# Performance work log

Hardware: AMD Instinct MI355X
Metric: run time of the kernel (lower is better)

Reference implementation:

```python
import jax, jax.numpy as jnp
import numpy as np

B = 16          # number of graphs in the batch (fixed for segment ops)
PTS = 4096      # points per graph
N = B * PTS
C = 256         # input feature channels
EPS = 1e-16     # PyG knn_interpolate eps


def setup_inputs() -> dict:
    key = jax.random.key(0)
    ks = jax.random.split(key, 12)
    x = jax.random.normal(ks[0], (N, C), dtype=jnp.float32)
    pos = jax.random.normal(ks[1], (N, 3), dtype=jnp.float32)
    x_skip = jax.random.normal(ks[2], (N, C), dtype=jnp.float32)
    pos_skip = jax.random.normal(ks[3], (N, 3), dtype=jnp.float32)
    # sorted segment ids, every graph populated
    batch = jnp.repeat(jnp.arange(B, dtype=jnp.int32), PTS)
    batch_skip = jnp.repeat(jnp.arange(B, dtype=jnp.int32), PTS)
    # MLP([C+3, 256, 512, 1024]) parameters (Linear + ReLU per layer)
    s = 0.02
    W1 = jax.random.normal(ks[4], (C + 3, 256), dtype=jnp.float32) * s
    b1 = jnp.zeros((256,), dtype=jnp.float32)
    W2 = jax.random.normal(ks[5], (256, 512), dtype=jnp.float32) * s
    b2 = jnp.zeros((512,), dtype=jnp.float32)
    W3 = jax.random.normal(ks[6], (512, 1024), dtype=jnp.float32) * s
    b3 = jnp.zeros((1024,), dtype=jnp.float32)
    return {"x": x, "pos": pos, "batch": batch, "x_skip": x_skip,
            "pos_skip": pos_skip, "batch_skip": batch_skip,
            "W1": W1, "b1": b1, "W2": W2, "b2": b2, "W3": W3, "b3": b3}


def reference(x, pos, batch, x_skip, pos_skip, batch_skip, W1, b1, W2, b2, W3, b3):
    # nn(cat([x, pos], dim=1)): 3-layer MLP with ReLU
    h = jnp.concatenate([x, pos], axis=1)            # [N, C+3]
    h = jax.nn.relu(h @ W1 + b1)                     # [N, 256]
    h = jax.nn.relu(h @ W2 + b2)                     # [N, 512]
    h = jax.nn.relu(h @ W3 + b3)                     # [N, 1024]
    # global_max_pool over each graph
    pooled = jax.ops.segment_max(h, batch, num_segments=B)  # [B, 1024]
    # knn_interpolate(pooled, origin-per-graph, pos_skip, k=3):
    # each graph contributes exactly ONE source point (the origin), so the
    # single in-batch neighbor gets inverse-distance weight that normalizes
    # to 1; written explicitly to mirror the PyG weighting math.
    d2 = jnp.sum(pos_skip * pos_skip, axis=1, keepdims=True)  # [Ns, 1] dist^2 to origin
    w = 1.0 / (d2 + EPS)
    gathered = pooled[batch_skip]                    # [Ns, 1024]
    interp = (w * gathered) / w                      # weights cancel -> gathered
    # cat with skip features
    out = jnp.concatenate([interp, x_skip], axis=1)  # [Ns, 1024 + C]
    return out
```

## Files before the change

### kernel.cpp

```cpp
#include <hip/hip_runtime.h>
#include <hip/hip_bf16.h>


typedef __attribute__((ext_vector_type(8))) short bf16x8;
typedef __attribute__((ext_vector_type(16))) float f32x16;

#define GLD_LDS16(src, dst) __builtin_amdgcn_global_load_lds( \
    (const __attribute__((address_space(1))) unsigned int*)(src), \
    (__attribute__((address_space(3))) unsigned int*)(dst), 16, 0, 0)

__device__ __forceinline__ unsigned short f2bf(float f) {
  unsigned int u = __float_as_uint(f);
  unsigned int r = (u + 0x7FFFu + ((u >> 16) & 1u)) >> 16;
  return (unsigned short)r;
}
__device__ __forceinline__ float bf2f(unsigned short h) {
  return __uint_as_float(((unsigned int)h) << 16);
}

__global__ void pack_a1(const float* __restrict__ x, const float* __restrict__ pos,
                        unsigned short* __restrict__ ah, unsigned short* __restrict__ al) {
  const int total = 65536 * 80;
  for (int idx = blockIdx.x * blockDim.x + threadIdx.x; idx < total;
       idx += gridDim.x * blockDim.x) {
    const int n = idx / 80;
    const int q = idx - n * 80;
    float4 v;
    if (q < 64) {
      v = ((const float4*)x)[(size_t)n * 64 + q];
    } else if (q == 64) {
      v.x = pos[(size_t)n * 3 + 0];
      v.y = pos[(size_t)n * 3 + 1];
      v.z = pos[(size_t)n * 3 + 2];
      v.w = 0.f;
    } else {
      v.x = v.y = v.z = v.w = 0.f;
    }
    ushort4 h, l;
    h.x = f2bf(v.x); l.x = f2bf(v.x - bf2f(h.x));
    h.y = f2bf(v.y); l.y = f2bf(v.y - bf2f(h.y));
    h.z = f2bf(v.z); l.z = f2bf(v.z - bf2f(h.z));
    h.w = f2bf(v.w); l.w = f2bf(v.w - bf2f(h.w));
    *(ushort4*)(ah + (size_t)n * 320 + q * 4) = h;
    *(ushort4*)(al + (size_t)n * 320 + q * 4) = l;
  }
}

__global__ void pack_w(const float* __restrict__ w, unsigned short* __restrict__ wh,
                       unsigned short* __restrict__ wl, int K, int Nout) {
  const int no = blockIdx.x;
  const int k = threadIdx.x;
  const int KP = blockDim.x;
  float v = (k < K) ? w[(size_t)k * Nout + no] : 0.f;
  unsigned short hi = f2bf(v);
  wh[(size_t)no * KP + k] = hi;
  wl[(size_t)no * KP + k] = f2bf(v - bf2f(hi));
}

__global__ void zero_pool(unsigned int* __restrict__ p) {
  p[blockIdx.x * 1024 + threadIdx.x] = 0u;
}

template<int KP, int NOUT, int MODE>
__global__ __launch_bounds__(256, 2)
void gemm_split(const unsigned short* __restrict__ gAh, const unsigned short* __restrict__ gAl,
                const unsigned short* __restrict__ gBh, const unsigned short* __restrict__ gBl,
                const float* __restrict__ bias,
                unsigned short* __restrict__ Ch, unsigned short* __restrict__ Cl,
                unsigned int* __restrict__ pooled, const int* __restrict__ batch) {
  constexpr int BM = 128, BN = 128, BK = 64;
  constexpr int NB = NOUT / BN;
  __shared__ unsigned short lds[4 * BM * BK];

  const int nwg = gridDim.x;
  const int bid = (blockIdx.x % 8) * (nwg / 8) + blockIdx.x / 8;
  const int bm = bid / NB, bn = bid % NB;
  const int r0 = bm * BM, c0 = bn * BN;
  const int tid = threadIdx.x;
  const int lane = tid & 63, wid = tid >> 6;
  const int wm = wid >> 1, wc = wid & 1;
  const int al31 = lane & 31, l5 = lane >> 5;
  const int swz = lane & 7, lr = lane >> 3;

  f32x16 acc[2][2] = {};

  const unsigned short* plane = (wid == 0) ? gAh : (wid == 1) ? gAl : (wid == 2) ? gBh : gBl;
  const int rb = (wid < 2) ? r0 : c0;
  unsigned short* sbase = lds + wid * (BM * BK);
  const unsigned short* gsrc0 = plane + (size_t)(rb + lr) * KP + ((swz ^ lr) << 3);
  unsigned short* ldst0 = sbase + lane * 8;

  for (int kt = 0; kt < KP / BK; ++kt) {
    {
      const unsigned short* s = gsrc0 + kt * BK;
      unsigned short* d = ldst0;
      #pragma unroll
      for (int t = 0; t < 16; ++t) {
        GLD_LDS16(s, d);
        s += 8 * KP;
        d += 512;
      }
    }
    __syncthreads();

    const unsigned short* sA_h = lds;
    const unsigned short* sA_l = lds + BM * BK;
    const unsigned short* sB_h = lds + 2 * BM * BK;
    const unsigned short* sB_l = lds + 3 * BM * BK;

    #pragma unroll
    for (int ks = 0; ks < BK / 16; ++ks) {
      bf16x8 fah[2], fal[2], fbh[2], fbl[2];
      const int cb = ks * 2 + l5;
      #pragma unroll
      for (int i = 0; i < 2; ++i) {
        const int arow = wm * 64 + i * 32 + al31;
        const int aoff = arow * BK + ((cb ^ (arow & 7)) << 3);
        fah[i] = *(const bf16x8*)(sA_h + aoff);
        fal[i] = *(const bf16x8*)(sA_l + aoff);
        const int brow = wc * 64 + i * 32 + al31;
        const int boff = brow * BK + ((cb ^ (brow & 7)) << 3);
        fbh[i] = *(const bf16x8*)(sB_h + boff);
        fbl[i] = *(const bf16x8*)(sB_l + boff);
      }
      #pragma unroll
      for (int i = 0; i < 2; ++i)
        #pragma unroll
        for (int j = 0; j < 2; ++j) {
          acc[i][j] = __builtin_amdgcn_mfma_f32_32x32x16_bf16(fah[i], fbh[j], acc[i][j], 0, 0, 0);
          acc[i][j] = __builtin_amdgcn_mfma_f32_32x32x16_bf16(fah[i], fbl[j], acc[i][j], 0, 0, 0);
          acc[i][j] = __builtin_amdgcn_mfma_f32_32x32x16_bf16(fal[i], fbh[j], acc[i][j], 0, 0, 0);
        }
    }
    __syncthreads();
  }

  if (MODE == 0) {
    #pragma unroll
    for (int i = 0; i < 2; ++i) {
      const int rbase = r0 + wm * 64 + i * 32 + 4 * l5;
      #pragma unroll
      for (int j = 0; j < 2; ++j) {
        const int col = c0 + wc * 64 + j * 32 + al31;
        const float bz = bias[col];
        #pragma unroll
        for (int r = 0; r < 16; ++r) {
          const int row = rbase + (r & 3) + 8 * (r >> 2);
          float v = fmaxf(acc[i][j][r] + bz, 0.f);
          unsigned short hi = f2bf(v);
          Ch[(size_t)row * NOUT + col] = hi;
          Cl[(size_t)row * NOUT + col] = f2bf(v - bf2f(hi));
        }
      }
    }
  } else {
    const int g = batch[r0];
    float* pb = (float*)lds;
    #pragma unroll
    for (int j = 0; j < 2; ++j) {
      const int colw = wc * 64 + j * 32 + al31;
      const float bz = bias[c0 + colw];
      float cm = 0.f;
      #pragma unroll
      for (int i = 0; i < 2; ++i)
        #pragma unroll
        for (int r = 0; r < 16; ++r)
          cm = fmaxf(cm, acc[i][j][r] + bz);
      cm = fmaxf(cm, __shfl_xor(cm, 32));
      if (l5 == 0) pb[wm * 128 + colw] = cm;
    }
    __syncthreads();
    if (tid < 128) {
      float m = fmaxf(pb[tid], pb[128 + tid]);
      atomicMax(pooled + (size_t)g * 1024 + c0 + tid, __float_as_uint(m));
    }
  }
}

__global__ void write_out(const float* __restrict__ pooled, const float* __restrict__ x_skip,
                          const int* __restrict__ batch_skip, float* __restrict__ out,
                          int N) {
  const int t = threadIdx.x;
  for (int n = blockIdx.x; n < N; n += gridDim.x) {
    const int g = batch_skip[n];
    const float4* ps = (const float4*)(pooled + (size_t)g * 1024);
    float4* o = (float4*)(out + (size_t)n * 1280);
    o[t] = ps[t];
    if (t < 64) {
      const float4* xs = (const float4*)(x_skip + (size_t)n * 256);
      o[256 + t] = xs[t];
    }
  }
}

extern "C" void kernel_launch(void* const* d_in, const int* in_sizes, int n_in,
                              void* d_out, int out_size, void* d_ws, size_t ws_size,
                              hipStream_t stream) {
  const float* x        = (const float*)d_in[0];
  const float* pos      = (const float*)d_in[1];
  const int*   batch    = (const int*)d_in[2];
  const float* x_skip   = (const float*)d_in[3];
  const int*   batch_sk = (const int*)d_in[5];
  const float* W1 = (const float*)d_in[6];
  const float* b1 = (const float*)d_in[7];
  const float* W2 = (const float*)d_in[8];
  const float* b2 = (const float*)d_in[9];
  const float* W3 = (const float*)d_in[10];
  const float* b3 = (const float*)d_in[11];
  float* out = (float*)d_out;

  char* ws = (char*)d_ws;
  unsigned short* a1h = (unsigned short*)(ws);
  unsigned short* a1l = (unsigned short*)(ws + 41943040);
  unsigned short* h2h = (unsigned short*)(ws);
  unsigned short* h2l = (unsigned short*)(ws + 67108864);
  size_t off = 134217728;
  unsigned short* h1h = (unsigned short*)(ws + off); off += 33554432;
  unsigned short* h1l = (unsigned short*)(ws + off); off += 33554432;
  unsigned short* w1h = (unsigned short*)(ws + off); off += 163840;
  unsigned short* w1l = (unsigned short*)(ws + off); off += 163840;
  unsigned short* w2h = (unsigned short*)(ws + off); off += 262144;
  unsigned short* w2l = (unsigned short*)(ws + off); off += 262144;
  unsigned short* w3h = (unsigned short*)(ws + off); off += 1048576;
  unsigned short* w3l = (unsigned short*)(ws + off); off += 1048576;
  unsigned int*  pooled = (unsigned int*)(ws + off);

  hipLaunchKernelGGL(pack_w, dim3(256),  dim3(320), 0, stream, W1, w1h, w1l, 259, 256);
  hipLaunchKernelGGL(pack_w, dim3(512),  dim3(256), 0, stream, W2, w2h, w2l, 256, 512);
  hipLaunchKernelGGL(pack_w, dim3(1024), dim3(512), 0, stream, W3, w3h, w3l, 512, 1024);
  hipLaunchKernelGGL(pack_a1, dim3(2048), dim3(256), 0, stream, x, pos, a1h, a1l);
  hipLaunchKernelGGL(zero_pool, dim3(16), dim3(1024), 0, stream, pooled);

  hipLaunchKernelGGL((gemm_split<320, 256, 0>), dim3(512 * 2), dim3(256), 0, stream,
                     a1h, a1l, w1h, w1l, b1, h1h, h1l,
                     (unsigned int*)nullptr, (const int*)nullptr);
  hipLaunchKernelGGL((gemm_split<256, 512, 0>), dim3(512 * 4), dim3(256), 0, stream,
                     h1h, h1l, w2h, w2l, b2, h2h, h2l,
                     (unsigned int*)nullptr, (const int*)nullptr);
  hipLaunchKernelGGL((gemm_split<512, 1024, 1>), dim3(512 * 8), dim3(256), 0, stream,
                     h2h, h2l, w3h, w3l, b3,
                     (unsigned short*)nullptr, (unsigned short*)nullptr, pooled, batch);

  hipLaunchKernelGGL(write_out, dim3(4096), dim3(256), 0, stream,
                     (const float*)pooled, x_skip, batch_sk, out, 65536);
}
```

Baseline: 771.1 us.

## Double-buffer split-bf16 GEMM LDS loads with 128x256 tiles and 512 threads

Restructures the split-precision GEMM kernel into a two-stage LDS double buffer: the next K-slice is loaded by global-to-LDS copies while the current slice feeds MFMA, which removes one barrier per iteration and overlaps memory with compute. The tile grows to 128x256 with BK=32 and 8 waves per block, so more output is computed per loaded A tile. The first layer's padded K also drops from 320 to 288 to cut wasted MFMA work. In exchange, per-iteration K depth is smaller, so there are more iterations and barriers, and LDS usage and register pressure rise.

New measurement: 820.8 us. 1.06x slower.

```diff
diff --git a/kernel.cpp b/kernel.cpp
--- a/kernel.cpp
+++ b/kernel.cpp
@@ -20,11 +20,11 @@
 
 __global__ void pack_a1(const float* __restrict__ x, const float* __restrict__ pos,
                         unsigned short* __restrict__ ah, unsigned short* __restrict__ al) {
-  const int total = 65536 * 80;
+  const int total = 65536 * 72;
   for (int idx = blockIdx.x * blockDim.x + threadIdx.x; idx < total;
        idx += gridDim.x * blockDim.x) {
-    const int n = idx / 80;
-    const int q = idx - n * 80;
+    const int n = idx / 72;
+    const int q = idx - n * 72;
     float4 v;
     if (q < 64) {
       v = ((const float4*)x)[(size_t)n * 64 + q];
@@ -41,8 +41,8 @@
     h.y = f2bf(v.y); l.y = f2bf(v.y - bf2f(h.y));
     h.z = f2bf(v.z); l.z = f2bf(v.z - bf2f(h.z));
     h.w = f2bf(v.w); l.w = f2bf(v.w - bf2f(h.w));
-    *(ushort4*)(ah + (size_t)n * 320 + q * 4) = h;
-    *(ushort4*)(al + (size_t)n * 320 + q * 4) = l;
+    *(ushort4*)(ah + (size_t)n * 288 + q * 4) = h;
+    *(ushort4*)(al + (size_t)n * 288 + q * 4) = l;
   }
 }
 
@@ -62,15 +62,17 @@
 }
 
 template<int KP, int NOUT, int MODE>
-__global__ __launch_bounds__(256, 2)
+__global__ __launch_bounds__(512, 2)
 void gemm_split(const unsigned short* __restrict__ gAh, const unsigned short* __restrict__ gAl,
                 const unsigned short* __restrict__ gBh, const unsigned short* __restrict__ gBl,
                 const float* __restrict__ bias,
                 unsigned short* __restrict__ Ch, unsigned short* __restrict__ Cl,
                 unsigned int* __restrict__ pooled, const int* __restrict__ batch) {
-  constexpr int BM = 128, BN = 128, BK = 64;
+  constexpr int BM = 128, BN = 256, BK = 32;
   constexpr int NB = NOUT / BN;
-  __shared__ unsigned short lds[4 * BM * BK];
+  constexpr int KT = KP / BK;
+  constexpr int BUF = 24576;
+  __shared__ unsigned short lds[2 * BUF];
 
   const int nwg = gridDim.x;
   const int bid = (blockIdx.x % 8) * (nwg / 8) + blockIdx.x / 8;
@@ -78,48 +80,60 @@
   const int r0 = bm * BM, c0 = bn * BN;
   const int tid = threadIdx.x;
   const int lane = tid & 63, wid = tid >> 6;
-  const int wm = wid >> 1, wc = wid & 1;
+  const int wm = wid >> 2, wn = wid & 3;
   const int al31 = lane & 31, l5 = lane >> 5;
-  const int swz = lane & 7, lr = lane >> 3;
+  const int lr = lane >> 2, swz = lane & 3;
 
   f32x16 acc[2][2] = {};
 
-  const unsigned short* plane = (wid == 0) ? gAh : (wid == 1) ? gAl : (wid == 2) ? gBh : gBl;
-  const int rb = (wid < 2) ? r0 : c0;
-  unsigned short* sbase = lds + wid * (BM * BK);
-  const unsigned short* gsrc0 = plane + (size_t)(rb + lr) * KP + ((swz ^ lr) << 3);
-  unsigned short* ldst0 = sbase + lane * 8;
-
-  for (int kt = 0; kt < KP / BK; ++kt) {
-    {
-      const unsigned short* s = gsrc0 + kt * BK;
-      unsigned short* d = ldst0;
-      #pragma unroll
-      for (int t = 0; t < 16; ++t) {
-        GLD_LDS16(s, d);
-        s += 8 * KP;
-        d += 512;
+  const unsigned short* src[6];
+  int dstoff[6];
+  #pragma unroll
+  for (int t = 0; t < 6; ++t) {
+    const int c = wid * 6 + t;
+    const unsigned short* pl; int rowb;
+    if (c < 8)       { pl = gAh; rowb = r0 + c * 16; }
+    else if (c < 16) { pl = gAl; rowb = r0 + (c - 8) * 16; }
+    else if (c < 32) { pl = gBh; rowb = c0 + (c - 16) * 16; }
+    else             { pl = gBl; rowb = c0 + (c - 32) * 16; }
+    src[t] = pl + (size_t)(rowb + lr) * KP + ((swz ^ (lr & 3)) << 3);
+    dstoff[t] = c * 512 + lane * 8;
+  }
+
+  #pragma unroll
+  for (int t = 0; t < 6; ++t) {
+    GLD_LDS16(src[t], lds + dstoff[t]);
+    src[t] += BK;
+  }
+  __syncthreads();
+
+  int cur = 0;
+  for (int kt = 0; kt < KT; ++kt) {
+    if (kt + 1 < KT) {
+      unsigned short* nb = lds + (cur ^ 1) * BUF;
+      #pragma unroll
+      for (int t = 0; t < 6; ++t) {
+        GLD_LDS16(src[t], nb + dstoff[t]);
+        src[t] += BK;
       }
     }
-    __syncthreads();
-
-    const unsigned short* sA_h = lds;
-    const unsigned short* sA_l = lds + BM * BK;
-    const unsigned short* sB_h = lds + 2 * BM * BK;
-    const unsigned short* sB_l = lds + 3 * BM * BK;
+    const unsigned short* sA_h = lds + cur * BUF;
+    const unsigned short* sA_l = sA_h + 4096;
+    const unsigned short* sB_h = sA_h + 8192;
+    const unsigned short* sB_l = sA_h + 16384;
 
     #pragma unroll
-    for (int ks = 0; ks < BK / 16; ++ks) {
+    for (int ks = 0; ks < 2; ++ks) {
       bf16x8 fah[2], fal[2], fbh[2], fbl[2];
       const int cb = ks * 2 + l5;
       #pragma unroll
       for (int i = 0; i < 2; ++i) {
         const int arow = wm * 64 + i * 32 + al31;
-        const int aoff = arow * BK + ((cb ^ (arow & 7)) << 3);
+        const int aoff = arow * BK + ((cb ^ (arow & 3)) << 3);
         fah[i] = *(const bf16x8*)(sA_h + aoff);
         fal[i] = *(const bf16x8*)(sA_l + aoff);
-        const int brow = wc * 64 + i * 32 + al31;
-        const int boff = brow * BK + ((cb ^ (brow & 7)) << 3);
+        const int brow = wn * 64 + i * 32 + al31;
+        const int boff = brow * BK + ((cb ^ (brow & 3)) << 3);
         fbh[i] = *(const bf16x8*)(sB_h + boff);
         fbl[i] = *(const bf16x8*)(sB_l + boff);
       }
@@ -133,6 +147,7 @@
         }
     }
     __syncthreads();
+    cur ^= 1;
   }
 
   if (MODE == 0) {
@@ -141,7 +156,7 @@
       const int rbase = r0 + wm * 64 + i * 32 + 4 * l5;
       #pragma unroll
       for (int j = 0; j < 2; ++j) {
-        const int col = c0 + wc * 64 + j * 32 + al31;
+        const int col = c0 + wn * 64 + j * 32 + al31;
         const float bz = bias[col];
         #pragma unroll
         for (int r = 0; r < 16; ++r) {
@@ -158,7 +173,7 @@
     float* pb = (float*)lds;
     #pragma unroll
     for (int j = 0; j < 2; ++j) {
-      const int colw = wc * 64 + j * 32 + al31;
+      const int colw = wn * 64 + j * 32 + al31;
       const float bz = bias[c0 + colw];
       float cm = 0.f;
       #pragma unroll
@@ -167,11 +182,11 @@
         for (int r = 0; r < 16; ++r)
           cm = fmaxf(cm, acc[i][j][r] + bz);
       cm = fmaxf(cm, __shfl_xor(cm, 32));
-      if (l5 == 0) pb[wm * 128 + colw] = cm;
+      if (l5 == 0) pb[wm * 256 + colw] = cm;
     }
     __syncthreads();
-    if (tid < 128) {
-      float m = fmaxf(pb[tid], pb[128 + tid]);
+    if (tid < 256) {
+      float m = fmaxf(pb[tid], pb[256 + tid]);
       atomicMax(pooled + (size_t)g * 1024 + c0 + tid, __float_as_uint(m));
     }
   }
@@ -217,27 +232,27 @@
   size_t off = 134217728;
   unsigned short* h1h = (unsigned short*)(ws + off); off += 33554432;
   unsigned short* h1l = (unsigned short*)(ws + off); off += 33554432;
-  unsigned short* w1h = (unsigned short*)(ws + off); off += 163840;
-  unsigned short* w1l = (unsigned short*)(ws + off); off += 163840;
+  unsigned short* w1h = (unsigned short*)(ws + off); off += 147456;
+  unsigned short* w1l = (unsigned short*)(ws + off); off += 147456;
   unsigned short* w2h = (unsigned short*)(ws + off); off += 262144;
   unsigned short* w2l = (unsigned short*)(ws + off); off += 262144;
   unsigned short* w3h = (unsigned short*)(ws + off); off += 1048576;
   unsigned short* w3l = (unsigned short*)(ws + off); off += 1048576;
   unsigned int*  pooled = (unsigned int*)(ws + off);
 
-  hipLaunchKernelGGL(pack_w, dim3(256),  dim3(320), 0, stream, W1, w1h, w1l, 259, 256);
+  hipLaunchKernelGGL(pack_w, dim3(256),  dim3(288), 0, stream, W1, w1h, w1l, 259, 256);
   hipLaunchKernelGGL(pack_w, dim3(512),  dim3(256), 0, stream, W2, w2h, w2l, 256, 512);
   hipLaunchKernelGGL(pack_w, dim3(1024), dim3(512), 0, stream, W3, w3h, w3l, 512, 1024);
   hipLaunchKernelGGL(pack_a1, dim3(2048), dim3(256), 0, stream, x, pos, a1h, a1l);
   hipLaunchKernelGGL(zero_pool, dim3(16), dim3(1024), 0, stream, pooled);
 
-  hipLaunchKernelGGL((gemm_split<320, 256, 0>), dim3(512 * 2), dim3(256), 0, stream,
+  hipLaunchKernelGGL((gemm_split<288, 256, 0>), dim3(512), dim3(512), 0, stream,
                      a1h, a1l, w1h, w1l, b1, h1h, h1l,
                      (unsigned int*)nullptr, (const int*)nullptr);
-  hipLaunchKernelGGL((gemm_split<256, 512, 0>), dim3(512 * 4), dim3(256), 0, stream,
+  hipLaunchKernelGGL((gemm_split<256, 512, 0>), dim3(1024), dim3(512), 0, stream,
                      h1h, h1l, w2h, w2l, b2, h2h, h2l,
                      (unsigned int*)nullptr, (const int*)nullptr);
-  hipLaunchKernelGGL((gemm_split<512, 1024, 1>), dim3(512 * 8), dim3(256), 0, stream,
+  hipLaunchKernelGGL((gemm_split<512, 1024, 1>), dim3(2048), dim3(512), 0, stream,
                      h2h, h2l, w3h, w3l, b3,
                      (unsigned short*)nullptr, (unsigned short*)nullptr, pooled, batch);
 
```
